# Optimization experiments

Hardware: AMD Instinct MI355X
Metric: run time of the kernel (lower is better)

The kernel has to match this reference:

```python
import jax, jax.numpy as jnp
import numpy as np

D_IN = 2048
D_SAE = 16384
BATCH = 4096


def setup_inputs() -> dict:
    key = jax.random.key(0)
    kx, kw, kb, kt, kd = jax.random.split(key, 5)
    x = jax.random.normal(kx, (BATCH, D_IN), dtype=jnp.float32)
    # kaiming-uniform-like init for encoder weight [d_sae, d_in]
    bound = float(np.sqrt(6.0 / D_IN))
    W_enc = jax.random.uniform(kw, (D_SAE, D_IN), minval=-bound, maxval=bound, dtype=jnp.float32)
    b_enc = jnp.zeros((D_SAE,), dtype=jnp.float32)
    # decoder weight [d_in, d_sae]; use small random values instead of the
    # zeros init so the reference output is non-degenerate
    W_dec = jax.random.normal(kd, (D_IN, D_SAE), dtype=jnp.float32) * 0.02
    # learnable per-feature thresholds tau (tau_init=0.0 plus jitter)
    tau = jax.random.normal(kt, (D_SAE,), dtype=jnp.float32) * 0.01
    return {"x": x, "W_enc": W_enc, "b_enc": b_enc, "tau": tau, "W_dec": W_dec, "k_cap": 64}


def reference(x, W_enc, b_enc, tau, W_dec, k_cap):
    # encode: pre = x @ W_enc.T + b_enc  -> [B, d_sae]
    pre = jnp.einsum('bi,si->bs', x, W_enc) + b_enc
    # JumpReLU gate: y = relu(pre - tau), mask = (pre > tau)
    codes = jax.nn.relu(pre - tau)
    mask = (pre > tau).astype(pre.dtype)
    # top-k cap (gate_mode='jumprelu_cap'): keep codes >= k-th largest per row
    k = min(k_cap, codes.shape[1])
    vals = jax.lax.top_k(codes, k)[0]          # [B, k], sorted desc
    kth = vals[:, -1:]                          # [B, 1]
    mask_k = (codes >= kth).astype(codes.dtype)
    codes = codes * mask_k
    mask = mask * mask_k
    # decode: recon = codes @ W_dec.T  -> [B, d_in]
    recon = jnp.einsum('bs,is->bi', codes, W_dec)
    return recon, codes, mask
```

## Files before the change

kernel.cpp:

```cpp
#include <hip/hip_runtime.h>

#define D_IN   2048
#define D_SAE  16384
#define BATCH  4096
#define CAP    256
#define MAXB   64
#define DELTA  1e-2f

typedef __attribute__((ext_vector_type(8))) _Float16 f16x8;
typedef __attribute__((ext_vector_type(4))) _Float16 f16x4;
typedef __attribute__((ext_vector_type(4))) float f32x4;

__global__ __launch_bounds__(256) void to_f16(const float* __restrict__ in,
                                              ushort* __restrict__ out, int n4) {
    int i = blockIdx.x * blockDim.x + threadIdx.x;
    int stride = gridDim.x * blockDim.x;
    for (; i < n4; i += stride) {
        float4 v = ((const float4*)in)[i];
        ushort4 h;
        float*  vp = (float*)&v;
        ushort* hp = (ushort*)&h;
        #pragma unroll
        for (int j = 0; j < 4; ++j) {
            _Float16 f = (_Float16)vp[j];
            hp[j] = *(ushort*)&f;
        }
        ((ushort4*)out)[i] = h;
    }
}

__device__ __forceinline__ void async_copy16(const void* g, void* l) {
    __builtin_amdgcn_global_load_lds(
        (const __attribute__((address_space(1))) unsigned int*)g,
        (__attribute__((address_space(3))) unsigned int*)l, 16, 0, 0);
}

template<int F16OUT>
__global__ __launch_bounds__(512) void gemm_enc_mfma(
        const ushort* __restrict__ xh,
        const ushort* __restrict__ wh,
        const float* __restrict__ b_enc,
        const float* __restrict__ tau,
        void* __restrict__ rawout) {
    __shared__ ushort lds[2][2][2][8192];

    const int tid  = threadIdx.x;
    const int w    = tid >> 6;
    const int lane = tid & 63;
    const int wm   = w >> 2;
    const int wn   = w & 3;
    const int m0 = blockIdx.x * 256;
    const int s0 = blockIdx.y * 256;

    const int fr = lane & 15;
    const int fq = lane >> 4;

    const int srow0 = w * 8 + (lane >> 3);
    const int srow1 = 64 + srow0;
    const int sc0i  = (((lane & 7) - srow0) & 7) * 8;

    const ushort* panelA = xh + (size_t)m0 * 2048;
    const ushort* panelB = wh + (size_t)s0 * 2048;

    auto stage_half = [&](int bufi, int ab, int h, int koff) {
        const ushort* gp = (ab == 0) ? panelA : panelB;
        const ushort* g0 = gp + (size_t)(h * 128 + srow0) * 2048 + koff + sc0i;
        const ushort* g1 = gp + (size_t)(h * 128 + srow1) * 2048 + koff + sc0i;
        async_copy16(g0, &lds[bufi][ab][h][w * 512]);
        async_copy16(g1, &lds[bufi][ab][h][4096 + w * 512]);
    };

    int a_off[8][2], b_off[4][2];
    #pragma unroll
    for (int m = 0; m < 8; ++m) {
        int r = m * 16 + fr;
        #pragma unroll
        for (int kk = 0; kk < 2; ++kk)
            a_off[m][kk] = r * 64 + (((kk * 4 + fq) + r) & 7) * 8;
    }
    #pragma unroll
    for (int g = 0; g < 4; ++g) {
        int r = (wn & 1) * 64 + g * 16 + fr;
        #pragma unroll
        for (int kk = 0; kk < 2; ++kk)
            b_off[g][kk] = r * 64 + (((kk * 4 + fq) + r) & 7) * 8;
    }

    f32x4 acc[8][4] = {};

    stage_half(0, 0, 0, 0);
    stage_half(0, 0, 1, 0);
    stage_half(0, 1, 0, 0);
    stage_half(0, 1, 1, 0);
    asm volatile("s_waitcnt vmcnt(0)" ::: "memory");
    asm volatile("s_barrier" ::: "memory");

#define PHASE(QM, QN, AB, H)                                                   \
    do {                                                                       \
        if (t < 31) stage_half(nbuf, AB, H, knext);                            \
        f16x8 af[4][2], bf[2][2];                                              \
        _Pragma("unroll") for (int mm = 0; mm < 4; ++mm)                       \
            _Pragma("unroll") for (int kk = 0; kk < 2; ++kk)                   \
                af[mm][kk] = *(const f16x8*)&ldsA[a_off[(QM) * 4 + mm][kk]];   \
        _Pragma("unroll") for (int nn = 0; nn < 2; ++nn)                       \
            _Pragma("unroll") for (int kk = 0; kk < 2; ++kk)                   \
                bf[nn][kk] = *(const f16x8*)&ldsB[b_off[(QN) * 2 + nn][kk]];   \
        asm volatile("s_barrier" ::: "memory");                                \
        __builtin_amdgcn_s_setprio(1);                                         \
        _Pragma("unroll") for (int kk = 0; kk < 2; ++kk)                       \
            _Pragma("unroll") for (int mm = 0; mm < 4; ++mm)                   \
                _Pragma("unroll") for (int nn = 0; nn < 2; ++nn)               \
                    acc[(QM) * 4 + mm][(QN) * 2 + nn] =                        \
                        __builtin_amdgcn_mfma_f32_16x16x32_f16(                \
                            af[mm][kk], bf[nn][kk],                            \
                            acc[(QM) * 4 + mm][(QN) * 2 + nn], 0, 0, 0);       \
        __builtin_amdgcn_s_setprio(0);                                         \
        asm volatile("s_barrier" ::: "memory");                                \
    } while (0)

    for (int t = 0; t < 32; ++t) {
        const int cbuf = t & 1, nbuf = cbuf ^ 1;
        const int knext = (t + 1) * 64;
        const ushort* ldsA = &lds[cbuf][0][wm][0];
        const ushort* ldsB = &lds[cbuf][1][wn >> 1][0];
        PHASE(0, 0, 0, 0);
        PHASE(0, 1, 0, 1);
        PHASE(1, 0, 1, 0);
        PHASE(1, 1, 1, 1);
        asm volatile("s_waitcnt vmcnt(0)" ::: "memory");
        asm volatile("s_barrier" ::: "memory");
    }
#undef PHASE

    float bias[4];
    int col[4];
    #pragma unroll
    for (int n = 0; n < 4; ++n) {
        col[n] = s0 + wn * 64 + n * 16 + fr;
        bias[n] = b_enc[col[n]] - tau[col[n]];
    }
    #pragma unroll
    for (int m = 0; m < 8; ++m) {
        int rbase = m0 + wm * 128 + m * 16 + fq * 4;
        #pragma unroll
        for (int n = 0; n < 4; ++n) {
            #pragma unroll
            for (int r = 0; r < 4; ++r) {
                float v = fmaxf(acc[m][n][r] + bias[n], 0.f);
                size_t ofs = (size_t)(rbase + r) * D_SAE + col[n];
                if (F16OUT) {
                    _Float16 hv = (_Float16)v;
                    ((ushort*)rawout)[ofs] = *(ushort*)&hv;
                } else {
                    ((float*)rawout)[ofs] = v;
                }
            }
        }
    }
}

__global__ __launch_bounds__(256) void transpose_wdec_f16(const float* __restrict__ W_dec,
                                                          _Float16* __restrict__ W_decT) {
    __shared__ float t[64][65];
    const int tid = threadIdx.x;
    const int x0 = blockIdx.x * 64;
    const int y0 = blockIdx.y * 64;
    const int tx = tid & 15;
    const int ty = tid >> 4;
    #pragma unroll
    for (int p = 0; p < 4; ++p) {
        float4 v = *(const float4*)&W_dec[(size_t)(y0 + p * 16 + ty) * D_SAE + x0 + tx * 4];
        t[p * 16 + ty][tx * 4 + 0] = v.x;
        t[p * 16 + ty][tx * 4 + 1] = v.y;
        t[p * 16 + ty][tx * 4 + 2] = v.z;
        t[p * 16 + ty][tx * 4 + 3] = v.w;
    }
    __syncthreads();
    #pragma unroll
    for (int p = 0; p < 4; ++p) {
        int s = p * 16 + ty;
        f16x4 o;
        #pragma unroll
        for (int q = 0; q < 4; ++q)
            o[q] = (_Float16)t[tx * 4 + q][s];
        *(f16x4*)&W_decT[(size_t)(x0 + s) * D_IN + y0 + tx * 4] = o;
    }
}

template<int SRC16>
__global__ __launch_bounds__(256) void select_apply(
        const void* __restrict__ rawsrc,
        float* __restrict__ codes, float* __restrict__ mask,
        const int* __restrict__ kptr,
        const float* __restrict__ x, const float* __restrict__ W_enc,
        const float* __restrict__ b_enc, const float* __restrict__ tau,
        int* __restrict__ cnt_out, int* __restrict__ idx_out,
        float* __restrict__ val_out) {
    const int row = blockIdx.x;
    const int tid = threadIdx.x;
    const long base = (long)row * D_SAE;

    float c[8][8];
    if (SRC16) {
        const ushort* rh = (const ushort*)rawsrc;
        #pragma unroll
        for (int i = 0; i < 8; ++i) {
            uint4 u = *(const uint4*)(rh + base + i * 2048 + tid * 8);
            const unsigned* up = (const unsigned*)&u;
            #pragma unroll
            for (int q = 0; q < 4; ++q) {
                ushort b0 = (ushort)(up[q] & 0xFFFFu), b1 = (ushort)(up[q] >> 16);
                _Float16 h0, h1;
                *(ushort*)&h0 = b0; *(ushort*)&h1 = b1;
                c[i][2 * q]     = (float)h0;
                c[i][2 * q + 1] = (float)h1;
            }
        }
    } else {
        const float* rf = (const float*)rawsrc;
        #pragma unroll
        for (int i = 0; i < 8; ++i) {
            float4 v0 = *(const float4*)(rf + base + i * 2048 + tid * 8);
            float4 v1 = *(const float4*)(rf + base + i * 2048 + tid * 8 + 4);
            c[i][0] = v0.x; c[i][1] = v0.y; c[i][2] = v0.z; c[i][3] = v0.w;
            c[i][4] = v1.x; c[i][5] = v1.y; c[i][6] = v1.z; c[i][7] = v1.w;
        }
    }

    int K = kptr[0];
    if (K > D_SAE) K = D_SAE;

    __shared__ int    hist[1024];
    __shared__ int    scan[256];
    __shared__ int    wsum[4];
    __shared__ int    bidx[MAXB];
    __shared__ double exactv[MAXB];
    __shared__ int    selfl[MAXB];
    __shared__ double dsum[4];
    __shared__ int    sh_B, sh_nAB, sh_kpat;

    #pragma unroll
    for (int q = 0; q < 4; ++q) hist[tid + q * 256] = 0;
    if (tid == 0) { sh_B = -1; sh_nAB = 0; }
    __syncthreads();
    #pragma unroll
    for (int i = 0; i < 8; ++i)
        #pragma unroll
        for (int j = 0; j < 8; ++j) {
            _Float16 h = (_Float16)c[i][j];
            ushort pat = *(ushort*)&h;
            if (pat) atomicAdd(&hist[pat >> 6], 1);
        }
    __syncthreads();

    int s_loc = hist[4 * tid] + hist[4 * tid + 1] + hist[4 * tid + 2] + hist[4 * tid + 3];
    const int my = 255 - tid;
    scan[my] = s_loc;
    __syncthreads();
    #pragma unroll
    for (int off = 1; off < 256; off <<= 1) {
        int a = scan[my];
        int b = (my >= off) ? scan[my - off] : 0;
        __syncthreads();
        scan[my] = a + b;
        __syncthreads();
    }
    int I = scan[my];
    int E = I - s_loc;
    if (I >= K && E < K) {
        int cnt = E, b;
        for (b = 4 * tid + 3; b > 4 * tid; --b) {
            cnt += hist[b];
            if (cnt >= K) break;
        }
        if (cnt < K) { cnt += hist[4 * tid]; b = 4 * tid; }
        sh_B = b;
        sh_nAB = cnt - hist[b];
    }
    __syncthreads();
    const int B = sh_B, nAB = sh_nAB;

    if (tid < 64) hist[tid] = 0;
    __syncthreads();
    if (B >= 0) {
        #pragma unroll
        for (int i = 0; i < 8; ++i)
            #pragma unroll
            for (int j = 0; j < 8; ++j) {
                _Float16 h = (_Float16)c[i][j];
                ushort pat = *(ushort*)&h;
                if (pat && (int)(pat >> 6) == B) atomicAdd(&hist[pat & 63], 1);
            }
    }
    __syncthreads();
    if (tid == 0) {
        int kpat = 0;
        if (B >= 0) {
            int cnt = nAB, l;
            for (l = 63; l >= 0; --l) {
                cnt += hist[l];
                if (cnt >= K) break;
            }
            if (l < 0) l = 0;
            kpat = (B << 6) | l;
        }
        sh_kpat = kpat;
    }
    __syncthreads();
    _Float16 kh; *(ushort*)&kh = (ushort)sh_kpat;
    const float kf = (float)kh;
    const float thr_hi = kf + DELTA;
    const float thr_lo = kf - DELTA;

    int cA = 0, cB2 = 0;
    #pragma unroll
    for (int i = 0; i < 8; ++i)
        #pragma unroll
        for (int j = 0; j < 8; ++j) {
            float cc = c[i][j];
            cA  += (cc > thr_hi);
            cB2 += (cc >= thr_lo) && (cc <= thr_hi);
        }
    {
        int a = cA;
        #pragma unroll
        for (int off = 32; off; off >>= 1) a += __shfl_xor(a, off, 64);
        if ((tid & 63) == 0) wsum[tid >> 6] = a;
    }
    __syncthreads();
    const int nA = wsum[0] + wsum[1] + wsum[2] + wsum[3];
    __syncthreads();

    scan[tid] = cB2;
    __syncthreads();
    #pragma unroll
    for (int off = 1; off < 256; off <<= 1) {
        int a = scan[tid];
        int b = (tid >= off) ? scan[tid - off] : 0;
        __syncthreads();
        scan[tid] = a + b;
        __syncthreads();
    }
    int posB = scan[tid] - cB2;
    int nb   = scan[255];
    if (nb > MAXB) nb = MAXB;

    {
        int p = posB;
        #pragma unroll
        for (int i = 0; i < 8; ++i)
            #pragma unroll
            for (int j = 0; j < 8; ++j) {
                float cc = c[i][j];
                if ((cc >= thr_lo) && (cc <= thr_hi)) {
                    if (p < MAXB) bidx[p] = i * 2048 + tid * 8 + j;
                    ++p;
                }
            }
    }
    __syncthreads();

    const float* xrow = x + (size_t)row * D_IN;
    for (int jj = 0; jj < nb; ++jj) {
        int s = bidx[jj];
        const float* wrow = W_enc + (size_t)s * D_IN;
        double a = 0.0;
        #pragma unroll
        for (int q = 0; q < 8; ++q)
            a += (double)xrow[tid * 8 + q] * (double)wrow[tid * 8 + q];
        #pragma unroll
        for (int off = 32; off; off >>= 1) a += __shfl_xor(a, off, 64);
        if ((tid & 63) == 0) dsum[tid >> 6] = a;
        __syncthreads();
        if (tid == 0)
            exactv[jj] = dsum[0] + dsum[1] + dsum[2] + dsum[3]
                         + (double)b_enc[s] - (double)tau[s];
        __syncthreads();
    }

    int m = K - nA;
    if (m > nb) m = nb;
    if (tid < nb) {
        double e = exactv[tid];
        int rank = 0;
        for (int l = 0; l < nb; ++l) rank += (exactv[l] > e);
        selfl[tid] = (rank < m) ? 1 : 0;
    }
    __syncthreads();

    unsigned long long ov = 0ull;
    for (int jj = 0; jj < nb; ++jj) {
        int s = bidx[jj];
        if (((s >> 3) & 255) == tid && selfl[jj])
            ov |= 1ull << (((s >> 11) << 3) | (s & 7));
    }

    int kc = 0;
    #pragma unroll
    for (int i = 0; i < 8; ++i)
        #pragma unroll
        for (int j = 0; j < 8; ++j) {
            float cc = c[i][j];
            bool sel = (cc > thr_hi) || ((ov >> (i * 8 + j)) & 1ull);
            kc += sel && (cc > 0.f);
        }
    __syncthreads();
    scan[tid] = kc;
    __syncthreads();
    #pragma unroll
    for (int off = 1; off < 256; off <<= 1) {
        int a = scan[tid];
        int b = (tid >= off) ? scan[tid - off] : 0;
        __syncthreads();
        scan[tid] = a + b;
        __syncthreads();
    }
    int pos   = scan[tid] - kc;
    int total = scan[255];

    #pragma unroll
    for (int i = 0; i < 8; ++i) {
        f32x4 cf0, cf1, mf0, mf1;
        #pragma unroll
        for (int j = 0; j < 8; ++j) {
            float cc = c[i][j];
            bool sel = (cc > thr_hi) || ((ov >> (i * 8 + j)) & 1ull);
            bool m_  = sel && (cc > 0.f);
            float cv = sel ? cc : 0.f;
            float mv = m_ ? 1.f : 0.f;
            if (j < 4) { cf0[j] = cv; mf0[j] = mv; }
            else       { cf1[j - 4] = cv; mf1[j - 4] = mv; }
            if (m_) {
                if (pos < CAP) {
                    idx_out[row * CAP + pos] = i * 2048 + tid * 8 + j;
                    val_out[row * CAP + pos] = cv;
                }
                ++pos;
            }
        }
        long o = base + i * 2048 + tid * 8;
        __builtin_nontemporal_store(cf0, (f32x4*)(codes + o));
        __builtin_nontemporal_store(cf1, (f32x4*)(codes + o + 4));
        __builtin_nontemporal_store(mf0, (f32x4*)(mask + o));
        __builtin_nontemporal_store(mf1, (f32x4*)(mask + o + 4));
    }
    if (tid == 0) cnt_out[row] = total < CAP ? total : CAP;
}

__global__ __launch_bounds__(256) void recon_sparse(const _Float16* __restrict__ Wd16,
                                                    const int* __restrict__ cnt,
                                                    const int* __restrict__ idx,
                                                    const float* __restrict__ val,
                                                    float* __restrict__ recon) {
    const int row  = blockIdx.x >> 1;
    const int half = blockIdx.x & 1;
    const int tid  = threadIdx.x;
    __shared__ int   s_idx[CAP];
    __shared__ float s_val[CAP];
    const int n = cnt[row];
    for (int j = tid; j < n; j += 256) {
        s_idx[j] = idx[row * CAP + j];
        s_val[j] = val[row * CAP + j];
    }
    __syncthreads();

    const int colb = half * 1024 + tid * 4;
    float4 a = {0.f, 0.f, 0.f, 0.f};
    for (int j = 0; j < n; ++j) {
        float c = s_val[j];
        f16x4 w0 = *(const f16x4*)(Wd16 + (size_t)s_idx[j] * D_IN + colb);
        a.x = fmaf(c, (float)w0[0], a.x); a.y = fmaf(c, (float)w0[1], a.y);
        a.z = fmaf(c, (float)w0[2], a.z); a.w = fmaf(c, (float)w0[3], a.w);
    }
    *(float4*)(recon + (size_t)row * D_IN + colb) = a;
}

extern "C" void kernel_launch(void* const* d_in, const int* in_sizes, int n_in,
                              void* d_out, int out_size, void* d_ws, size_t ws_size,
                              hipStream_t stream) {
    const float* x     = (const float*)d_in[0];
    const float* W_enc = (const float*)d_in[1];
    const float* b_enc = (const float*)d_in[2];
    const float* tau   = (const float*)d_in[3];
    const float* W_dec = (const float*)d_in[4];
    const int*   kptr  = (const int*)d_in[5];

    float* recon = (float*)d_out;
    float* codes = recon + (size_t)BATCH * D_IN;
    float* maskp = codes + (size_t)BATCH * D_SAE;

    char* w = (char*)d_ws;
    const size_t OFF_X   = (size_t)D_SAE * D_IN * 2;
    const size_t OFF_RAW = OFF_X + (size_t)BATCH * D_IN * 2;
    const size_t RAWSZ   = (size_t)BATCH * D_SAE * 2;
    const size_t TAILSZ  = 16384 + 2 * (size_t)BATCH * CAP * 4;
    const bool f16raw = ws_size >= OFF_RAW + RAWSZ + TAILSZ;

    const size_t OFF_CNT = f16raw ? (OFF_RAW + RAWSZ) : OFF_RAW;
    ushort*   w_f16  = (ushort*)w;
    ushort*   x_f16  = (ushort*)(w + OFF_X);
    _Float16* W_decT = (_Float16*)w;
    int*      cnt    = (int*)  (w + OFF_CNT);
    int*      idxl   = (int*)  (w + OFF_CNT + 16384);
    float*    vall   = (float*)(w + OFF_CNT + 16384 + (size_t)BATCH * CAP * 4);
    void*     raw    = f16raw ? (void*)(w + OFF_RAW) : (void*)codes;

    hipLaunchKernelGGL(to_f16, dim3(1024), dim3(256), 0, stream,
                       x, x_f16, BATCH * D_IN / 4);
    hipLaunchKernelGGL(to_f16, dim3(4096), dim3(256), 0, stream,
                       W_enc, w_f16, D_SAE * D_IN / 4);
    if (f16raw) {
        hipLaunchKernelGGL((gemm_enc_mfma<1>), dim3(BATCH / 256, D_SAE / 256), dim3(512), 0, stream,
                           x_f16, w_f16, b_enc, tau, raw);
        hipLaunchKernelGGL((select_apply<1>), dim3(BATCH), dim3(256), 0, stream,
                           raw, codes, maskp, kptr, x, W_enc, b_enc, tau, cnt, idxl, vall);
    } else {
        hipLaunchKernelGGL((gemm_enc_mfma<0>), dim3(BATCH / 256, D_SAE / 256), dim3(512), 0, stream,
                           x_f16, w_f16, b_enc, tau, raw);
        hipLaunchKernelGGL((select_apply<0>), dim3(BATCH), dim3(256), 0, stream,
                           raw, codes, maskp, kptr, x, W_enc, b_enc, tau, cnt, idxl, vall);
    }
    hipLaunchKernelGGL(transpose_wdec_f16, dim3(D_SAE / 64, D_IN / 64), dim3(256), 0, stream,
                       W_dec, W_decT);
    hipLaunchKernelGGL(recon_sparse, dim3(BATCH * 2), dim3(256), 0, stream,
                       W_decT, cnt, idxl, vall, recon);
}
```

Before: 700.9 us.

## Replace double-buffered LDS staging with a nine-slot rolling ring pipeline

The encoder GEMM used two full LDS buffers and drained all outstanding loads with vmcnt(0) plus a barrier at the end of every k-step. It now keeps a ring of nine 16 KB slots and issues one half-tile load per phase, about five units ahead of use. A partial vmcnt(4) wait then lets loads stay in flight across k-steps instead of stalling on them. The cost is more LDS (144 KB versus 128 KB), which may limit occupancy, plus modulo-9 slot arithmetic and trickier ordering between barriers and loads.

```diff
diff --git a/kernel.cpp b/kernel.cpp
--- a/kernel.cpp
+++ b/kernel.cpp
@@ -42,7 +42,7 @@
         const float* __restrict__ b_enc,
         const float* __restrict__ tau,
         void* __restrict__ rawout) {
-    __shared__ ushort lds[2][2][2][8192];
+    __shared__ ushort lds9[9][8192];
 
     const int tid  = threadIdx.x;
     const int w    = tid >> 6;
@@ -62,12 +62,12 @@
     const ushort* panelA = xh + (size_t)m0 * 2048;
     const ushort* panelB = wh + (size_t)s0 * 2048;
 
-    auto stage_half = [&](int bufi, int ab, int h, int koff) {
+    auto stage_unit = [&](int slot, int ab, int h, int koff) {
         const ushort* gp = (ab == 0) ? panelA : panelB;
         const ushort* g0 = gp + (size_t)(h * 128 + srow0) * 2048 + koff + sc0i;
         const ushort* g1 = gp + (size_t)(h * 128 + srow1) * 2048 + koff + sc0i;
-        async_copy16(g0, &lds[bufi][ab][h][w * 512]);
-        async_copy16(g1, &lds[bufi][ab][h][4096 + w * 512]);
+        async_copy16(g0, &lds9[slot][w * 512]);
+        async_copy16(g1, &lds9[slot][4096 + w * 512]);
     };
 
     int a_off[8][2], b_off[4][2];
@@ -88,16 +88,33 @@
 
     f32x4 acc[8][4] = {};
 
-    stage_half(0, 0, 0, 0);
-    stage_half(0, 0, 1, 0);
-    stage_half(0, 1, 0, 0);
-    stage_half(0, 1, 1, 0);
-    asm volatile("s_waitcnt vmcnt(0)" ::: "memory");
-    asm volatile("s_barrier" ::: "memory");
-
-#define PHASE(QM, QN, AB, H)                                                   \
+    stage_unit(0, 0, 0, 0);
+    stage_unit(1, 1, 0, 0);
+    stage_unit(2, 1, 1, 0);
+    stage_unit(3, 0, 1, 0);
+    stage_unit(4, 0, 0, 64);
+
+    const int wmu = wm ? 3 : 0;
+    const int wbu = 1 + (wn >> 1);
+
+#define STG(P)                                                                 \
     do {                                                                       \
-        if (t < 31) stage_half(nbuf, AB, H, knext);                            \
+        int u_ = 4 * t + (P) + 5;                                              \
+        if (u_ < 128) {                                                        \
+            int ui_ = u_ & 3;                                                  \
+            stage_unit(u_ % 9, (ui_ == 0 || ui_ == 3) ? 0 : 1,                 \
+                       (ui_ >= 2) ? 1 : 0, (u_ >> 2) * 64);                    \
+        }                                                                      \
+    } while (0)
+
+#define PHASE(QM, QN, P)                                                       \
+    do {                                                                       \
+        STG(P);                                                                \
+        if ((P) == 0) {                                                        \
+            if (t != 31) asm volatile("s_waitcnt vmcnt(4)" ::: "memory");      \
+            else         asm volatile("s_waitcnt vmcnt(0)" ::: "memory");      \
+        }                                                                      \
+        asm volatile("s_barrier" ::: "memory");                                \
         f16x8 af[4][2], bf[2][2];                                              \
         _Pragma("unroll") for (int mm = 0; mm < 4; ++mm)                       \
             _Pragma("unroll") for (int kk = 0; kk < 2; ++kk)                   \
@@ -105,7 +122,6 @@
         _Pragma("unroll") for (int nn = 0; nn < 2; ++nn)                       \
             _Pragma("unroll") for (int kk = 0; kk < 2; ++kk)                   \
                 bf[nn][kk] = *(const f16x8*)&ldsB[b_off[(QN) * 2 + nn][kk]];   \
-        asm volatile("s_barrier" ::: "memory");                                \
         __builtin_amdgcn_s_setprio(1);                                         \
         _Pragma("unroll") for (int kk = 0; kk < 2; ++kk)                       \
             _Pragma("unroll") for (int mm = 0; mm < 4; ++mm)                   \
@@ -119,18 +135,15 @@
     } while (0)
 
     for (int t = 0; t < 32; ++t) {
-        const int cbuf = t & 1, nbuf = cbuf ^ 1;
-        const int knext = (t + 1) * 64;
-        const ushort* ldsA = &lds[cbuf][0][wm][0];
-        const ushort* ldsB = &lds[cbuf][1][wn >> 1][0];
-        PHASE(0, 0, 0, 0);
-        PHASE(0, 1, 0, 1);
-        PHASE(1, 0, 1, 0);
-        PHASE(1, 1, 1, 1);
-        asm volatile("s_waitcnt vmcnt(0)" ::: "memory");
-        asm volatile("s_barrier" ::: "memory");
+        const ushort* ldsA = &lds9[(4 * t + wmu) % 9][0];
+        const ushort* ldsB = &lds9[(4 * t + wbu) % 9][0];
+        PHASE(0, 0, 0);
+        PHASE(0, 1, 1);
+        PHASE(1, 0, 2);
+        PHASE(1, 1, 3);
     }
 #undef PHASE
+#undef STG
 
     float bias[4];
     int col[4];
```

New measurement: 700.1 us. Within noise of the previous version (-0.1%).
